# Optimization experiments

Measured on AMD Instinct MI355X. Metric: run time of the kernel, lower is better.

Reference implementation:

```python
import jax, jax.numpy as jnp
import numpy as np

EVAL_NUM = 6          # self.eval_num
NMS_THRESHOLD = 2.0   # self.nms_threshold


def _nms_single(coords, scores, trajs):
    """Greedy goals_NMS for one sample.
    coords: [N, 2] goal positions, scores: [N], trajs: [N, T, 2].
    Returns (sel_goals [K,2], sel_probs [K], sel_trajs [K,T,2]) with K=EVAL_NUM.
    """
    N = scores.shape[0]
    K = EVAL_NUM
    thr2 = jnp.asarray(NMS_THRESHOLD, scores.dtype) ** 2

    order = jnp.argsort(-scores)           # descending score
    c = coords[order]                      # [N, 2]
    s = scores[order]                      # [N]
    t = trajs[order]                       # [N, T, 2]

    slots = jnp.arange(K)

    def step(carry, j):
        sel_pts, sel_idx, count = carry
        pt = c[j]                                        # [2]
        d2 = jnp.sum((sel_pts - pt) ** 2, axis=-1)       # [K]
        active = slots < count
        conflict = jnp.any(active & (d2 < thr2))
        accept = (count < K) & (~conflict)
        slot = (slots == count) & accept                 # one-hot write position
        sel_pts = jnp.where(slot[:, None], pt, sel_pts)
        sel_idx = jnp.where(slot, j, sel_idx)
        count = count + accept.astype(count.dtype)
        return (sel_pts, sel_idx, count), None

    init = (jnp.zeros((K, 2), coords.dtype), jnp.zeros((K,), jnp.int32), jnp.int32(0))
    (sel_pts, sel_idx, _), _ = jax.lax.scan(step, init, jnp.arange(N))
    return sel_pts, s[sel_idx], t[sel_idx]


def setup_inputs() -> dict:
    key = jax.random.key(0)
    k1, k2, k3, k4 = jax.random.split(key, 4)
    B, N, T = 256, 4096, 30
    return {
        "outputs_coord": jax.random.normal(k1, (B, 1, N, 2), dtype=jnp.float32) * 20.0,
        "outputs_class": jax.random.uniform(k2, (B, 1, N), dtype=jnp.float32),
        "outputs_traj": jax.random.normal(k3, (B, 1, N, T, 2), dtype=jnp.float32),
        "outputs_centerness": jax.random.uniform(k4, (B, 1, N), dtype=jnp.float32),
    }


def reference(outputs_coord, outputs_class, outputs_traj, outputs_centerness):
    # eval path of Decoder_predict.forward: per-sample score = class * centerness,
    # then greedy NMS over goals to pick eval_num trajectories.
    coords = outputs_coord[:, 0]                           # [B, N, 2]
    scores = outputs_class[:, 0] * outputs_centerness[:, 0]  # [B, N]
    trajs = outputs_traj[:, 0]                             # [B, N, T, 2]
    goals, probs, pred_trajs = jax.vmap(_nms_single)(coords, scores, trajs)
    # pred_trajs_batch [B, 6, T, 2], pred_probs_batch [B, 6], goals [B, 6, 2]
    return pred_trajs, probs, goals
```

## Files before the change

### kernel.cpp

```cpp
#include <hip/hip_runtime.h>
#include <hip/hip_bf16.h>

#define BATCH 256
#define NPTS  4096
#define TLEN  30
#define KSEL  6

__global__ __launch_bounds__(256)
void nms_kernel(const float* __restrict__ coord,
                const float* __restrict__ cls,
                const float* __restrict__ traj,
                const float* __restrict__ cent,
                float* __restrict__ out)
{
    const int b   = blockIdx.x;
    const int tid = threadIdx.x;

    __shared__ float s_scores[NPTS];
    __shared__ float w_v[4];
    __shared__ int   w_i[4];
    __shared__ float s_selx[KSEL], s_sely[KSEL], s_selscore[KSEL];
    __shared__ int   s_selidx[KSEL];
    __shared__ int   s_count, s_done, s_firstidx;
    __shared__ float s_firstscore;

    const float* cls_b   = cls   + (size_t)b * NPTS;
    const float* cent_b  = cent  + (size_t)b * NPTS;
    const float* coord_b = coord + (size_t)b * NPTS * 2;

    for (int i = tid; i < NPTS; i += 256)
        s_scores[i] = cls_b[i] * cent_b[i];

    if (tid == 0) { s_count = 0; s_done = 0; s_firstidx = 0; s_firstscore = 0.0f; }
    __syncthreads();

    for (int iter = 0; iter < NPTS; ++iter) {
        float bv = -2.0f;
        int   bi = NPTS;
        for (int i = tid; i < NPTS; i += 256) {
            float v = s_scores[i];
            if (v > bv || (v == bv && i < bi)) { bv = v; bi = i; }
        }
        for (int off = 32; off > 0; off >>= 1) {
            float ov = __shfl_down(bv, off, 64);
            int   oi = __shfl_down(bi, off, 64);
            if (ov > bv || (ov == bv && oi < bi)) { bv = ov; bi = oi; }
        }
        const int wave = tid >> 6, lane = tid & 63;
        if (lane == 0) { w_v[wave] = bv; w_i[wave] = bi; }
        __syncthreads();

        if (tid == 0) {
            bv = w_v[0]; bi = w_i[0];
            #pragma unroll
            for (int w = 1; w < 4; ++w) {
                if (w_v[w] > bv || (w_v[w] == bv && w_i[w] < bi)) { bv = w_v[w]; bi = w_i[w]; }
            }
            if (bv < 0.0f) {
                s_done = 1;
            } else {
                s_scores[bi] = -1.0f;
                if (iter == 0) { s_firstidx = bi; s_firstscore = bv; }
                const float px = coord_b[2 * bi];
                const float py = coord_b[2 * bi + 1];
                bool conflict = false;
                const int cnt = s_count;
                for (int k = 0; k < cnt; ++k) {
                    const float dx = s_selx[k] - px;
                    const float dy = s_sely[k] - py;
                    if (dx * dx + dy * dy < 4.0f) conflict = true;
                }
                if (!conflict) {
                    s_selx[cnt] = px; s_sely[cnt] = py;
                    s_selscore[cnt] = bv; s_selidx[cnt] = bi;
                    s_count = cnt + 1;
                    if (cnt + 1 == KSEL) s_done = 1;
                }
            }
        }
        __syncthreads();
        if (s_done) break;
    }

    const int   cnt    = s_count;
    const int   fidx   = s_firstidx;
    const float fscore = s_firstscore;

    const float* traj_b   = traj + (size_t)b * NPTS * TLEN * 2;
    float*       out_traj = out  + (size_t)b * KSEL * TLEN * 2;
    for (int e = tid; e < KSEL * TLEN * 2; e += 256) {
        const int k = e / (TLEN * 2);
        const int j = e - k * (TLEN * 2);
        const int idx = (k < cnt) ? s_selidx[k] : fidx;
        out_traj[e] = traj_b[(size_t)idx * (TLEN * 2) + j];
    }

    float* out_probs = out + (size_t)BATCH * KSEL * TLEN * 2;
    if (tid < KSEL)
        out_probs[b * KSEL + tid] = (tid < cnt) ? s_selscore[tid] : fscore;

    float* out_goals = out + (size_t)BATCH * KSEL * TLEN * 2 + (size_t)BATCH * KSEL;
    if (tid >= 64 && tid < 64 + KSEL * 2) {
        const int e = tid - 64;
        const int k = e >> 1, d = e & 1;
        const float v = (k < cnt) ? (d ? s_sely[k] : s_selx[k]) : 0.0f;
        out_goals[(b * KSEL + k) * 2 + d] = v;
    }
}

extern "C" void kernel_launch(void* const* d_in, const int* in_sizes, int n_in,
                              void* d_out, int out_size, void* d_ws, size_t ws_size,
                              hipStream_t stream) {
    const float* coord = (const float*)d_in[0];
    const float* cls   = (const float*)d_in[1];
    const float* traj  = (const float*)d_in[2];
    const float* cent  = (const float*)d_in[3];
    float* out = (float*)d_out;

    nms_kernel<<<BATCH, 256, 0, stream>>>(coord, cls, traj, cent, out);
}
```

Measured before the change: 306.5 us.

## Use 1024 threads per block with register-held scores and float4 loads

Raises the block size from 256 to 1024 threads so each thread owns exactly four contiguous scores. The first argmax pass runs from registers, and later passes read scores with a single float4 LDS load instead of a 16-element strided loop. The initial barrier is dropped, and the trajectory gather now copies float4 elements. In exchange, the serial cross-wave reduction done by thread 0 grows from 4 to 16 entries, and each barrier now covers 16 waves.

```diff
diff --git a/kernel.cpp b/kernel.cpp
--- a/kernel.cpp
+++ b/kernel.cpp
@@ -5,8 +5,10 @@
 #define NPTS  4096
 #define TLEN  30
 #define KSEL  6
+#define THREADS 1024
+#define NWAVES (THREADS / 64)
 
-__global__ __launch_bounds__(256)
+__global__ __launch_bounds__(THREADS)
 void nms_kernel(const float* __restrict__ coord,
                 const float* __restrict__ cls,
                 const float* __restrict__ traj,
@@ -17,8 +19,8 @@
     const int tid = threadIdx.x;
 
     __shared__ float s_scores[NPTS];
-    __shared__ float w_v[4];
-    __shared__ int   w_i[4];
+    __shared__ float w_v[NWAVES];
+    __shared__ int   w_i[NWAVES];
     __shared__ float s_selx[KSEL], s_sely[KSEL], s_selscore[KSEL];
     __shared__ int   s_selidx[KSEL];
     __shared__ int   s_count, s_done, s_firstidx;
@@ -28,34 +30,45 @@
     const float* cent_b  = cent  + (size_t)b * NPTS;
     const float* coord_b = coord + (size_t)b * NPTS * 2;
 
-    for (int i = tid; i < NPTS; i += 256)
-        s_scores[i] = cls_b[i] * cent_b[i];
+    const float4 c4 = reinterpret_cast<const float4*>(cls_b)[tid];
+    const float4 e4 = reinterpret_cast<const float4*>(cent_b)[tid];
+    float p[4] = { c4.x * e4.x, c4.y * e4.y, c4.z * e4.z, c4.w * e4.w };
+    reinterpret_cast<float4*>(s_scores)[tid] = make_float4(p[0], p[1], p[2], p[3]);
 
     if (tid == 0) { s_count = 0; s_done = 0; s_firstidx = 0; s_firstscore = 0.0f; }
-    __syncthreads();
+
+    const int wave = tid >> 6, lane = tid & 63;
 
     for (int iter = 0; iter < NPTS; ++iter) {
-        float bv = -2.0f;
-        int   bi = NPTS;
-        for (int i = tid; i < NPTS; i += 256) {
-            float v = s_scores[i];
-            if (v > bv || (v == bv && i < bi)) { bv = v; bi = i; }
+        float bv;
+        int   bi;
+        if (iter == 0) {
+            bv = p[0]; bi = tid * 4;
+            #pragma unroll
+            for (int j = 1; j < 4; ++j)
+                if (p[j] > bv) { bv = p[j]; bi = tid * 4 + j; }
+        } else {
+            const float4 s4 = reinterpret_cast<const float4*>(s_scores)[tid];
+            const float q[4] = { s4.x, s4.y, s4.z, s4.w };
+            bv = q[0]; bi = tid * 4;
+            #pragma unroll
+            for (int j = 1; j < 4; ++j)
+                if (q[j] > bv) { bv = q[j]; bi = tid * 4 + j; }
         }
+        #pragma unroll
         for (int off = 32; off > 0; off >>= 1) {
-            float ov = __shfl_down(bv, off, 64);
-            int   oi = __shfl_down(bi, off, 64);
+            const float ov = __shfl_down(bv, off, 64);
+            const int   oi = __shfl_down(bi, off, 64);
             if (ov > bv || (ov == bv && oi < bi)) { bv = ov; bi = oi; }
         }
-        const int wave = tid >> 6, lane = tid & 63;
         if (lane == 0) { w_v[wave] = bv; w_i[wave] = bi; }
         __syncthreads();
 
         if (tid == 0) {
             bv = w_v[0]; bi = w_i[0];
             #pragma unroll
-            for (int w = 1; w < 4; ++w) {
+            for (int w = 1; w < NWAVES; ++w)
                 if (w_v[w] > bv || (w_v[w] == bv && w_i[w] < bi)) { bv = w_v[w]; bi = w_i[w]; }
-            }
             if (bv < 0.0f) {
                 s_done = 1;
             } else {
@@ -86,22 +99,24 @@
     const int   fidx   = s_firstidx;
     const float fscore = s_firstscore;
 
-    const float* traj_b   = traj + (size_t)b * NPTS * TLEN * 2;
-    float*       out_traj = out  + (size_t)b * KSEL * TLEN * 2;
-    for (int e = tid; e < KSEL * TLEN * 2; e += 256) {
-        const int k = e / (TLEN * 2);
-        const int j = e - k * (TLEN * 2);
+    const float4* traj_b4   = reinterpret_cast<const float4*>(traj + (size_t)b * NPTS * TLEN * 2);
+    float4*       out_traj4 = reinterpret_cast<float4*>(out + (size_t)b * KSEL * TLEN * 2);
+    if (tid < KSEL * 15) {
+        const int k = tid / 15;
+        const int j = tid - k * 15;
         const int idx = (k < cnt) ? s_selidx[k] : fidx;
-        out_traj[e] = traj_b[(size_t)idx * (TLEN * 2) + j];
+        out_traj4[tid] = traj_b4[(size_t)idx * 15 + j];
     }
 
     float* out_probs = out + (size_t)BATCH * KSEL * TLEN * 2;
-    if (tid < KSEL)
-        out_probs[b * KSEL + tid] = (tid < cnt) ? s_selscore[tid] : fscore;
+    if (tid >= 128 && tid < 128 + KSEL) {
+        const int k = tid - 128;
+        out_probs[b * KSEL + k] = (k < cnt) ? s_selscore[k] : fscore;
+    }
 
     float* out_goals = out + (size_t)BATCH * KSEL * TLEN * 2 + (size_t)BATCH * KSEL;
-    if (tid >= 64 && tid < 64 + KSEL * 2) {
-        const int e = tid - 64;
+    if (tid >= 192 && tid < 192 + KSEL * 2) {
+        const int e = tid - 192;
         const int k = e >> 1, d = e & 1;
         const float v = (k < cnt) ? (d ? s_sely[k] : s_selx[k]) : 0.0f;
         out_goals[(b * KSEL + k) * 2 + d] = v;
@@ -117,5 +132,5 @@
     const float* cent  = (const float*)d_in[3];
     float* out = (float*)d_out;
 
-    nms_kernel<<<BATCH, 256, 0, stream>>>(coord, cls, traj, cent, out);
+    nms_kernel<<<BATCH, THREADS, 0, stream>>>(coord, cls, traj, cent, out);
 }
```

New measurement: 302.3 us. About the same (-1.3%).
